# Kernel tuning notes

Measured on AMD Instinct MI355X. Metric: run time of the kernel, lower is better.

The kernel has to match this reference:

```python
import jax, jax.numpy as jnp
import numpy as np
import math

H = 12          # num_attention_heads
DH = 64         # attention_head_size
LN_EPS = 1e-5


def layer_norm(x, gamma, beta):
    mu = jnp.mean(x, axis=-1, keepdims=True)
    var = jnp.mean(jnp.square(x - mu), axis=-1, keepdims=True)
    return (x - mu) * jax.lax.rsqrt(var + LN_EPS) * gamma + beta


def setup_inputs() -> dict:
    key = jax.random.key(0)
    ks = jax.random.split(key, 12)
    B, Lq, Lk, D = 4, 512, 512, 768
    s = 1.0 / math.sqrt(D)
    return {
        "hidden_states": jax.random.normal(ks[0], (B, Lq, D), jnp.float32),
        "context": jax.random.normal(ks[1], (B, Lk, D), jnp.float32),
        "attention_mask": jnp.zeros((B, 1, 1, Lk), jnp.float32),
        "graph_arc": jax.random.randint(ks[2], (B, Lq, Lk), 0, 3, jnp.int32),
        "Wq": jax.random.normal(ks[3], (D, D), jnp.float32) * s,
        "bq": jnp.zeros((D,), jnp.float32),
        "Wk": jax.random.normal(ks[4], (D, D), jnp.float32) * s,
        "bk": jnp.zeros((D,), jnp.float32),
        "Wv": jax.random.normal(ks[5], (D, D), jnp.float32) * s,
        "bv": jnp.zeros((D,), jnp.float32),
        "dpk_emb": jax.random.normal(ks[6], (3, DH), jnp.float32),
        "dpv_emb": jax.random.normal(ks[7], (3, DH), jnp.float32),
        "lnk_g": jnp.ones((DH,), jnp.float32),
        "lnk_b": jnp.zeros((DH,), jnp.float32),
        "lnv_g": jnp.ones((DH,), jnp.float32),
        "lnv_b": jnp.zeros((DH,), jnp.float32),
    }


def reference(hidden_states, context, attention_mask, graph_arc,
              Wq, bq, Wk, bk, Wv, bv,
              dpk_emb, dpv_emb, lnk_g, lnk_b, lnv_g, lnv_b):
    B, Lq, D = hidden_states.shape
    Lk = context.shape[1]

    def heads(x, L):  # [B,L,D] -> [B,H,L,dh]
        return x.reshape(B, L, H, DH).transpose(0, 2, 1, 3)

    q = heads(hidden_states @ Wq + bq, Lq)
    k = heads(context @ Wk + bk, Lk)
    v = heads(context @ Wv + bv, Lk)

    # relation embeddings per (query, key) pair: [B,Lq,Lk,dh]
    dp_keys = layer_norm(dpk_emb[graph_arc], lnk_g, lnk_b)
    dp_values = layer_norm(dpv_emb[graph_arc], lnv_g, lnv_b)

    scores = jnp.einsum('bhqd,bhkd->bhqk', q, k) / math.sqrt(DH)
    scores = scores + jnp.einsum('bhqd,bqkd->bhqk', q, dp_keys)
    scores = scores + attention_mask
    probs = jax.nn.softmax(scores, axis=-1)  # dropout p=0.0 -> identity

    ctx = jnp.einsum('bhqk,bhkd->bhqd', probs, v)
    ctx = ctx + jnp.einsum('bhqk,bqkd->bhqd', probs, dp_values)
    ctx = ctx.transpose(0, 2, 1, 3).reshape(B, Lq, D)
    return ctx
```

## Files before the change

### kernel.cpp

```cpp
#include <hip/hip_runtime.h>
#include <hip/hip_fp16.h>

#define NB 4
#define NH 12
#define DHD 64
#define LQ 512
#define LK 512
#define DM 768

typedef __attribute__((ext_vector_type(4))) _Float16 f16x4;
typedef __attribute__((ext_vector_type(8))) _Float16 f16x8;
typedef __attribute__((ext_vector_type(4))) float f32x4;

typedef __attribute__((address_space(1))) const unsigned int ga_uint;
typedef __attribute__((address_space(3))) unsigned int lds_uint;
__device__ static inline void gload_lds16(const void* g, void* l) {
    __builtin_amdgcn_global_load_lds((ga_uint*)g, (lds_uint*)l, 16, 0, 0);
}

__global__ __launch_bounds__(256) void prep_kernel(
    const float* __restrict__ Wq, const float* __restrict__ Wk,
    const float* __restrict__ Wv,
    const float* __restrict__ dpk, const float* __restrict__ dpv,
    const float* __restrict__ gk, const float* __restrict__ bk,
    const float* __restrict__ gv, const float* __restrict__ bv,
    _Float16* __restrict__ WT, float* __restrict__ lnK, float* __restrict__ lnV)
{
    const int bid = blockIdx.x, t = threadIdx.x;
    if (bid < 432) {
        __shared__ float sT[64][65];
        int mat = bid / 144, tile = bid % 144;
        int k0 = (tile / 12) * 64, n0 = (tile % 12) * 64;
        const float* W = (mat == 0) ? Wq : (mat == 1) ? Wk : Wv;
        #pragma unroll
        for (int p = 0; p < 4; ++p) {
            int idx = t + p * 256;
            int ki = idx >> 4, nj = (idx & 15) * 4;
            float4 wv = *(const float4*)&W[(size_t)(k0 + ki) * DM + n0 + nj];
            sT[ki][nj + 0] = wv.x; sT[ki][nj + 1] = wv.y;
            sT[ki][nj + 2] = wv.z; sT[ki][nj + 3] = wv.w;
        }
        __syncthreads();
        _Float16* dst = WT + (size_t)mat * DM * DM;
        #pragma unroll
        for (int p = 0; p < 4; ++p) {
            int idx = t + p * 256;
            int nr = idx >> 4, kj = (idx & 15) * 4;
            f16x4 hv = { (_Float16)sT[kj + 0][nr], (_Float16)sT[kj + 1][nr],
                         (_Float16)sT[kj + 2][nr], (_Float16)sT[kj + 3][nr] };
            *(f16x4*)&dst[(size_t)(n0 + nr) * DM + k0 + kj] = hv;
        }
    } else if (t < 64) {
        int lane = t;
        for (int r = 0; r < 3; ++r) {
            {
                float x = dpk[r * DHD + lane];
                float s = x;
                #pragma unroll
                for (int o = 1; o < 64; o <<= 1) s += __shfl_xor(s, o);
                float mu = s * (1.0f / 64.0f);
                float d = x - mu;
                float v = d * d;
                #pragma unroll
                for (int o = 1; o < 64; o <<= 1) v += __shfl_xor(v, o);
                lnK[r * DHD + lane] =
                    (d * rsqrtf(v * (1.0f / 64.0f) + 1e-5f) * gk[lane] + bk[lane]) * 8.0f;
            }
            {
                float x = dpv[r * DHD + lane];
                float s = x;
                #pragma unroll
                for (int o = 1; o < 64; o <<= 1) s += __shfl_xor(s, o);
                float mu = s * (1.0f / 64.0f);
                float d = x - mu;
                float v = d * d;
                #pragma unroll
                for (int o = 1; o < 64; o <<= 1) v += __shfl_xor(v, o);
                lnV[r * DHD + lane] =
                    d * rsqrtf(v * (1.0f / 64.0f) + 1e-5f) * gv[lane] + bv[lane];
            }
        }
    }
}

__global__ __launch_bounds__(256) void qkv_mfma(
    const float* __restrict__ hidden, const float* __restrict__ context,
    const _Float16* __restrict__ WT,
    const float* __restrict__ bq, const float* __restrict__ bk,
    const float* __restrict__ bv,
    _Float16* __restrict__ Qh, _Float16* __restrict__ Kh,
    _Float16* __restrict__ VTh)
{
    __shared__ __align__(16) char smem[43008];
    _Float16 (*sA)[64][72] = (_Float16(*)[64][72])smem;
    _Float16 (*sC)[104] = (_Float16(*)[104])smem;
    _Float16 (*sCV)[72] = (_Float16(*)[72])smem;

    const int t = threadIdx.x;
    const int w = t >> 6, lane = t & 63, g = lane >> 4, c16 = lane & 15;
    const int wm = w >> 1, wn = w & 1;
    const int mat = blockIdx.y / 8, nt0 = blockIdx.y % 8;
    const int m0 = blockIdx.x * 64, n0 = nt0 * 96;
    const float* X     = (mat == 0) ? hidden : context;
    const _Float16* Wt = WT + (size_t)mat * DM * DM;
    const float* bias  = (mat == 0) ? bq : (mat == 1) ? bk : bv;

    const int srow  = lane >> 3;
    const int sunit = (lane & 7) ^ srow;

    #pragma unroll
    for (int p = 0; p < 4; ++p) {
        int idx = t + p * 256;
        int row = idx >> 4, c4 = idx & 15;
        float4 xv = *(const float4*)&X[(size_t)(m0 + row) * DM + c4 * 4];
        f16x4 hv = { (_Float16)xv.x, (_Float16)xv.y,
                     (_Float16)xv.z, (_Float16)xv.w };
        *(f16x4*)&sA[0][row][c4 * 4] = hv;
    }
    #pragma unroll
    for (int cc = 0; cc < 3; ++cc) {
        int chunk = w * 3 + cc;
        int row = chunk * 8 + srow;
        gload_lds16((const char*)&Wt[(size_t)(n0 + row) * DM] + sunit * 16,
                    smem + 18432 + chunk * 1024);
    }
    __syncthreads();

    f32x4 acc[2][3];
    #pragma unroll
    for (int mt = 0; mt < 2; ++mt)
        #pragma unroll
        for (int nt = 0; nt < 3; ++nt) acc[mt][nt] = (f32x4){0.f, 0.f, 0.f, 0.f};

    for (int kt = 0; kt < 12; ++kt) {
        const int cur = kt & 1, nxt = cur ^ 1;
        char* sBc = smem + 18432 + cur * 12288;
        char* sBn = smem + 18432 + nxt * 12288;
        float4 xv[4];
        if (kt < 11) {
            #pragma unroll
            for (int p = 0; p < 4; ++p) {
                int idx = t + p * 256;
                int row = idx >> 4, c4 = idx & 15;
                xv[p] = *(const float4*)&X[(size_t)(m0 + row) * DM + (kt + 1) * 64 + c4 * 4];
            }
            #pragma unroll
            for (int cc = 0; cc < 3; ++cc) {
                int chunk = w * 3 + cc;
                int row = chunk * 8 + srow;
                gload_lds16(
                    (const char*)&Wt[(size_t)(n0 + row) * DM + (kt + 1) * 64] + sunit * 16,
                    sBn + chunk * 1024);
            }
        }
        #pragma unroll
        for (int kh = 0; kh < 2; ++kh) {
            f16x8 af[2], bf[3];
            #pragma unroll
            for (int mt = 0; mt < 2; ++mt)
                af[mt] = *(const f16x8*)&sA[cur][wm * 32 + mt * 16 + c16][kh * 32 + 8 * g];
            #pragma unroll
            for (int nt = 0; nt < 3; ++nt) {
                int rn = wn * 48 + nt * 16 + c16;
                int boff = (rn * 128 + kh * 64 + g * 16) ^ ((rn & 7) << 4);
                bf[nt] = *(const f16x8*)(sBc + boff);
            }
            #pragma unroll
            for (int mt = 0; mt < 2; ++mt)
                #pragma unroll
                for (int nt = 0; nt < 3; ++nt)
                    acc[mt][nt] = __builtin_amdgcn_mfma_f32_16x16x32_f16(
                        af[mt], bf[nt], acc[mt][nt], 0, 0, 0);
        }
        if (kt < 11) {
            #pragma unroll
            for (int p = 0; p < 4; ++p) {
                int idx = t + p * 256;
                int row = idx >> 4, c4 = idx & 15;
                f16x4 hv = { (_Float16)xv[p].x, (_Float16)xv[p].y,
                             (_Float16)xv[p].z, (_Float16)xv[p].w };
                *(f16x4*)&sA[nxt][row][c4 * 4] = hv;
            }
        }
        __syncthreads();
    }

    const float sc = (mat == 0) ? 0.125f : 1.0f;
    float bb[3];
    #pragma unroll
    for (int nt = 0; nt < 3; ++nt)
        bb[nt] = bias[n0 + wn * 48 + nt * 16 + c16] * sc;
    __syncthreads();

    const int bbat = m0 >> 9, l0 = m0 & 511;
    if (mat < 2) {
        #pragma unroll
        for (int mt = 0; mt < 2; ++mt)
            #pragma unroll
            for (int nt = 0; nt < 3; ++nt)
                #pragma unroll
                for (int r = 0; r < 4; ++r)
                    sC[wm * 32 + mt * 16 + 4 * g + r][wn * 48 + nt * 16 + c16] =
                        (_Float16)(acc[mt][nt][r] * sc + bb[nt]);
        __syncthreads();
        _Float16* dst = (mat == 0) ? Qh : Kh;
        int row = t >> 2, qc = t & 3;
        #pragma unroll
        for (int j = 0; j < 3; ++j) {
            int col = qc * 24 + j * 8;
            int hd = (n0 + col) >> 6, d8 = (n0 + col) & 63;
            *(f16x8*)&dst[((size_t)(bbat * NH + hd) * LQ + l0 + row) * DHD + d8] =
                *(const f16x8*)&sC[row][col];
        }
    } else {
        #pragma unroll
        for (int mt = 0; mt < 2; ++mt)
            #pragma unroll
            for (int nt = 0; nt < 3; ++nt)
                #pragma unroll
                for (int r = 0; r < 4; ++r)
                    sCV[wn * 48 + nt * 16 + c16][wm * 32 + mt * 16 + 4 * g + r] =
                        (_Float16)(acc[mt][nt][r] + bb[nt]);
        __syncthreads();
        #pragma unroll
        for (int p = 0; p < 3; ++p) {
            int idx = t + p * 256;
            int n = idx >> 3, c8 = idx & 7;
            *(f16x8*)&VTh[((size_t)(bbat * NH + ((n0 + n) >> 6)) * DHD + ((n0 + n) & 63)) * LK
                          + l0 + c8 * 8] = *(const f16x8*)&sCV[n][c8 * 8];
        }
    }
}

__global__ __launch_bounds__(256) void attn_mfma(
    const _Float16* __restrict__ Qh, const _Float16* __restrict__ Kh,
    const _Float16* __restrict__ VTh, const float* __restrict__ maskp,
    const int* __restrict__ garc, const float* __restrict__ lnK,
    const float* __restrict__ lnV, float* __restrict__ outp)
{
    __shared__ __align__(16) _Float16 sP[32][520];
    __shared__ unsigned int sArcW[32 * 33];
    __shared__ float sTb[32][4];
    __shared__ float sMax[4][32];
    __shared__ float sFin[32][4];

    const int t = threadIdx.x;
    const int w = t >> 6, lane = t & 63, g = lane >> 4, c16 = lane & 15;
    const int bx = blockIdx.x;
    const int qt = bx & 15, h = (bx >> 4) % NH, b = bx / (16 * NH);
    const int q0 = qt * 32;
    const int kw = w * 128;

    const _Float16* Qb = Qh + ((size_t)(b * NH + h) * LQ) * DHD;
    const _Float16* Kb = Kh + ((size_t)(b * NH + h) * LK) * DHD;
    const _Float16* Vb = VTh + ((size_t)(b * NH + h) * DHD) * LK;

    if (t < 32) {
        sFin[t][0] = 0.f; sFin[t][1] = 0.f; sFin[t][2] = 0.f; sFin[t][3] = 0.f;
    }
    const int* garcRow = garc + ((size_t)(b * LQ + q0)) * LK;
    #pragma unroll
    for (int p = 0; p < 4; ++p) {
        int idx = t + p * 256;
        int row = idx >> 5, wd = idx & 31;
        const int4* src = (const int4*)&garcRow[idx * 16];
        unsigned int u = 0;
        #pragma unroll
        for (int j = 0; j < 4; ++j) {
            int4 a4 = src[j];
            u |= (unsigned int)a4.x << (j * 8 + 0);
            u |= (unsigned int)a4.y << (j * 8 + 2);
            u |= (unsigned int)a4.z << (j * 8 + 4);
            u |= (unsigned int)a4.w << (j * 8 + 6);
        }
        sArcW[row * 33 + wd] = u;
    }
    if (t < 192) {
        int q = t / 6, rem = t % 6, rr = rem >> 1, part = rem & 1;
        const _Float16* qp = Qb + (size_t)(q0 + q) * DHD + part * 32;
        const float* lp = lnK + rr * 64 + part * 32;
        float a = 0.f;
        #pragma unroll
        for (int j = 0; j < 4; ++j) {
            f16x8 qv = *(const f16x8*)&qp[j * 8];
            float4 l0 = *(const float4*)&lp[j * 8];
            float4 l1 = *(const float4*)&lp[j * 8 + 4];
            a += (float)qv[0] * l0.x + (float)qv[1] * l0.y
               + (float)qv[2] * l0.z + (float)qv[3] * l0.w
               + (float)qv[4] * l1.x + (float)qv[5] * l1.y
               + (float)qv[6] * l1.z + (float)qv[7] * l1.w;
        }
        a += __shfl_xor(a, 1);
        if (part == 0) sTb[q][rr] = a;
    }
    f16x8 qa[2][2];
    #pragma unroll
    for (int qg = 0; qg < 2; ++qg) {
        qa[qg][0] = *(const f16x8*)&Qb[(q0 + 16 * qg + c16) * DHD + 8 * g];
        qa[qg][1] = *(const f16x8*)&Qb[(q0 + 16 * qg + c16) * DHD + 32 + 8 * g];
    }
    __syncthreads();

    f32x4 c[8][2];
    unsigned int aPk[2][2] = {{0u, 0u}, {0u, 0u}};
    float rm[2][4];
    const int sh = c16 * 2;
    #pragma unroll
    for (int qg = 0; qg < 2; ++qg)
        #pragma unroll
        for (int r = 0; r < 4; ++r) rm[qg][r] = -1e30f;
    #pragma unroll
    for (int tt = 0; tt < 8; ++tt) {
        int kg = kw + tt * 16 + c16;
        f16x8 kb0 = *(const f16x8*)&Kb[kg * DHD + 8 * g];
        f16x8 kb1 = *(const f16x8*)&Kb[kg * DHD + 32 + 8 * g];
        float mv = maskp[b * LK + kg];
        const int wb = w * 8 + tt;
        #pragma unroll
        for (int qg = 0; qg < 2; ++qg) {
            f32x4 s = (f32x4){0.f, 0.f, 0.f, 0.f};
            s = __builtin_amdgcn_mfma_f32_16x16x32_f16(qa[qg][0], kb0, s, 0, 0, 0);
            s = __builtin_amdgcn_mfma_f32_16x16x32_f16(qa[qg][1], kb1, s, 0, 0, 0);
            #pragma unroll
            for (int r = 0; r < 4; ++r) {
                int qrow = 16 * qg + 4 * g + r;
                unsigned int a = (sArcW[qrow * 33 + wb] >> sh) & 3u;
                aPk[qg][tt >> 2] |= a << ((tt & 3) * 8 + 2 * r);
                float sv = s[r] + sTb[qrow][a] + mv;
                s[r] = sv;
                rm[qg][r] = fmaxf(rm[qg][r], sv);
            }
            c[tt][qg] = s;
        }
    }

    #pragma unroll
    for (int qg = 0; qg < 2; ++qg)
        #pragma unroll
        for (int r = 0; r < 4; ++r) {
            float m = rm[qg][r];
            m = fmaxf(m, __shfl_xor(m, 1));
            m = fmaxf(m, __shfl_xor(m, 2));
            m = fmaxf(m, __shfl_xor(m, 4));
            m = fmaxf(m, __shfl_xor(m, 8));
            rm[qg][r] = m;
        }
    if (c16 == 0)
        #pragma unroll
        for (int qg = 0; qg < 2; ++qg)
            #pragma unroll
            for (int r = 0; r < 4; ++r) sMax[w][16 * qg + 4 * g + r] = rm[qg][r];
    __syncthreads();
    float Mr[2][4];
    #pragma unroll
    for (int qg = 0; qg < 2; ++qg)
        #pragma unroll
        for (int r = 0; r < 4; ++r) {
            int q = 16 * qg + 4 * g + r;
            Mr[qg][r] = fmaxf(fmaxf(sMax[0][q], sMax[1][q]),
                              fmaxf(sMax[2][q], sMax[3][q]));
        }

    float b0s[2][4], b1s[2][4], b2s[2][4];
    #pragma unroll
    for (int qg = 0; qg < 2; ++qg)
        #pragma unroll
        for (int r = 0; r < 4; ++r) {
            b0s[qg][r] = 0.f; b1s[qg][r] = 0.f; b2s[qg][r] = 0.f;
        }
    #pragma unroll
    for (int tt = 0; tt < 8; ++tt) {
        int kg = kw + tt * 16 + c16;
        #pragma unroll
        for (int qg = 0; qg < 2; ++qg)
            #pragma unroll
            for (int r = 0; r < 4; ++r) {
                float e = __expf(c[tt][qg][r] - Mr[qg][r]);
                unsigned int a = (aPk[qg][tt >> 2] >> ((tt & 3) * 8 + 2 * r)) & 3u;
                b0s[qg][r] += (a == 0u) ? e : 0.f;
                b1s[qg][r] += (a == 1u) ? e : 0.f;
                b2s[qg][r] += (a == 2u) ? e : 0.f;
                sP[16 * qg + 4 * g + r][kg] = (_Float16)e;
            }
    }
    #pragma unroll
    for (int qg = 0; qg < 2; ++qg)
        #pragma unroll
        for (int r = 0; r < 4; ++r) {
            #pragma unroll
            for (int o = 1; o < 16; o <<= 1) {
                b0s[qg][r] += __shfl_xor(b0s[qg][r], o);
                b1s[qg][r] += __shfl_xor(b1s[qg][r], o);
                b2s[qg][r] += __shfl_xor(b2s[qg][r], o);
            }
        }
    if (c16 == 0)
        #pragma unroll
        for (int qg = 0; qg < 2; ++qg)
            #pragma unroll
            for (int r = 0; r < 4; ++r) {
                int q = 16 * qg + 4 * g + r;
                atomicAdd(&sFin[q][0], b0s[qg][r]);
                atomicAdd(&sFin[q][1], b1s[qg][r]);
                atomicAdd(&sFin[q][2], b2s[qg][r]);
            }
    __syncthreads();

    f32x4 o[2] = {(f32x4){0.f, 0.f, 0.f, 0.f}, (f32x4){0.f, 0.f, 0.f, 0.f}};
    const _Float16* vrow = Vb + (size_t)(w * 16 + c16) * LK;
    #pragma unroll
    for (int ktile = 0; ktile < 16; ++ktile) {
        f16x8 vb = *(const f16x8*)&vrow[ktile * 32 + 8 * g];
        #pragma unroll
        for (int qg = 0; qg < 2; ++qg) {
            f16x8 pa = *(const f16x8*)&sP[16 * qg + c16][ktile * 32 + 8 * g];
            o[qg] = __builtin_amdgcn_mfma_f32_16x16x32_f16(pa, vb, o[qg], 0, 0, 0);
        }
    }

    int d = w * 16 + c16;
    float lv0 = lnV[d], lv1 = lnV[64 + d], lv2 = lnV[128 + d];
    #pragma unroll
    for (int qg = 0; qg < 2; ++qg)
        #pragma unroll
        for (int r = 0; r < 4; ++r) {
            int q = 16 * qg + 4 * g + r;
            float4 st = *(const float4*)&sFin[q][0];
            float inv = 1.0f / (st.x + st.y + st.z);
            float val = (o[qg][r] + st.x * lv0 + st.y * lv1 + st.z * lv2) * inv;
            outp[((size_t)(b * LQ + q0 + q)) * DM + h * DHD + d] = val;
        }
}

extern "C" void kernel_launch(void* const* d_in, const int* in_sizes, int n_in,
                              void* d_out, int out_size, void* d_ws, size_t ws_size,
                              hipStream_t stream) {
    const float* hidden  = (const float*)d_in[0];
    const float* context = (const float*)d_in[1];
    const float* mask    = (const float*)d_in[2];
    const int*   garc    = (const int*)d_in[3];
    const float* Wq = (const float*)d_in[4];
    const float* bq = (const float*)d_in[5];
    const float* Wk = (const float*)d_in[6];
    const float* bk = (const float*)d_in[7];
    const float* Wv = (const float*)d_in[8];
    const float* bv = (const float*)d_in[9];
    const float* dpk  = (const float*)d_in[10];
    const float* dpv  = (const float*)d_in[11];
    const float* lnkg = (const float*)d_in[12];
    const float* lnkb = (const float*)d_in[13];
    const float* lnvg = (const float*)d_in[14];
    const float* lnvb = (const float*)d_in[15];
    float* out = (float*)d_out;

    const size_t perT = (size_t)NB * NH * LQ * DHD;
    _Float16* Qh  = (_Float16*)d_ws;
    _Float16* Kh  = Qh + perT;
    _Float16* VTh = Kh + perT;
    _Float16* WT  = VTh + perT;
    float* lnK = (float*)(WT + (size_t)3 * DM * DM);
    float* lnV = lnK + 192;

    prep_kernel<<<433, 256, 0, stream>>>(Wq, Wk, Wv, dpk, dpv,
                                         lnkg, lnkb, lnvg, lnvb, WT, lnK, lnV);
    qkv_mfma<<<dim3(32, 24), 256, 0, stream>>>(hidden, context, WT,
                                               bq, bk, bv, Qh, Kh, VTh);
    attn_mfma<<<768, 256, 0, stream>>>(Qh, Kh, VTh, mask, garc, lnK, lnV, out);
}
```

Baseline: 138.5 us.

## Pre-pack graph arcs once and halve attention query tile to 16 rows

```diff
diff --git a/kernel.cpp b/kernel.cpp
--- a/kernel.cpp
+++ b/kernel.cpp
@@ -24,7 +24,9 @@
     const float* __restrict__ dpk, const float* __restrict__ dpv,
     const float* __restrict__ gk, const float* __restrict__ bk,
     const float* __restrict__ gv, const float* __restrict__ bv,
-    _Float16* __restrict__ WT, float* __restrict__ lnK, float* __restrict__ lnV)
+    const int* __restrict__ garc,
+    _Float16* __restrict__ WT, float* __restrict__ lnK, float* __restrict__ lnV,
+    unsigned int* __restrict__ arcP)
 {
     const int bid = blockIdx.x, t = threadIdx.x;
     if (bid < 432) {
@@ -50,35 +52,56 @@
                          (_Float16)sT[kj + 2][nr], (_Float16)sT[kj + 3][nr] };
             *(f16x4*)&dst[(size_t)(n0 + nr) * DM + k0 + kj] = hv;
         }
-    } else if (t < 64) {
-        int lane = t;
-        for (int r = 0; r < 3; ++r) {
-            {
-                float x = dpk[r * DHD + lane];
-                float s = x;
-                #pragma unroll
-                for (int o = 1; o < 64; o <<= 1) s += __shfl_xor(s, o);
-                float mu = s * (1.0f / 64.0f);
-                float d = x - mu;
-                float v = d * d;
-                #pragma unroll
-                for (int o = 1; o < 64; o <<= 1) v += __shfl_xor(v, o);
-                lnK[r * DHD + lane] =
-                    (d * rsqrtf(v * (1.0f / 64.0f) + 1e-5f) * gk[lane] + bk[lane]) * 8.0f;
-            }
-            {
-                float x = dpv[r * DHD + lane];
-                float s = x;
-                #pragma unroll
-                for (int o = 1; o < 64; o <<= 1) s += __shfl_xor(s, o);
-                float mu = s * (1.0f / 64.0f);
-                float d = x - mu;
-                float v = d * d;
-                #pragma unroll
-                for (int o = 1; o < 64; o <<= 1) v += __shfl_xor(v, o);
-                lnV[r * DHD + lane] =
-                    d * rsqrtf(v * (1.0f / 64.0f) + 1e-5f) * gv[lane] + bv[lane];
-            }
+    } else if (bid == 432) {
+        if (t < 64) {
+            int lane = t;
+            for (int r = 0; r < 3; ++r) {
+                {
+                    float x = dpk[r * DHD + lane];
+                    float s = x;
+                    #pragma unroll
+                    for (int o = 1; o < 64; o <<= 1) s += __shfl_xor(s, o);
+                    float mu = s * (1.0f / 64.0f);
+                    float d = x - mu;
+                    float v = d * d;
+                    #pragma unroll
+                    for (int o = 1; o < 64; o <<= 1) v += __shfl_xor(v, o);
+                    lnK[r * DHD + lane] =
+                        (d * rsqrtf(v * (1.0f / 64.0f) + 1e-5f) * gk[lane] + bk[lane]) * 8.0f;
+                }
+                {
+                    float x = dpv[r * DHD + lane];
+                    float s = x;
+                    #pragma unroll
+                    for (int o = 1; o < 64; o <<= 1) s += __shfl_xor(s, o);
+                    float mu = s * (1.0f / 64.0f);
+                    float d = x - mu;
+                    float v = d * d;
+                    #pragma unroll
+                    for (int o = 1; o < 64; o <<= 1) v += __shfl_xor(v, o);
+                    lnV[r * DHD + lane] =
+                        d * rsqrtf(v * (1.0f / 64.0f) + 1e-5f) * gv[lane] + bv[lane];
+                }
+            }
+        }
+    } else {
+        int pb = bid - 433;
+        #pragma unroll
+        for (int j = 0; j < 2; ++j) {
+            int wi = pb * 512 + t + j * 256;
+            int bq = wi >> 5;
+            int wd = wi & 31;
+            const int4* src = (const int4*)&garc[((size_t)bq * LK) + wd * 16];
+            unsigned int u = 0;
+            #pragma unroll
+            for (int k = 0; k < 4; ++k) {
+                int4 a4 = src[k];
+                u |= (unsigned int)a4.x << (k * 8 + 0);
+                u |= (unsigned int)a4.y << (k * 8 + 2);
+                u |= (unsigned int)a4.z << (k * 8 + 4);
+                u |= (unsigned int)a4.w << (k * 8 + 6);
+            }
+            arcP[wi] = u;
         }
     }
 }
@@ -235,47 +258,36 @@
 __global__ __launch_bounds__(256) void attn_mfma(
     const _Float16* __restrict__ Qh, const _Float16* __restrict__ Kh,
     const _Float16* __restrict__ VTh, const float* __restrict__ maskp,
-    const int* __restrict__ garc, const float* __restrict__ lnK,
+    const unsigned int* __restrict__ arcP, const float* __restrict__ lnK,
     const float* __restrict__ lnV, float* __restrict__ outp)
 {
-    __shared__ __align__(16) _Float16 sP[32][520];
-    __shared__ unsigned int sArcW[32 * 33];
-    __shared__ float sTb[32][4];
-    __shared__ float sMax[4][32];
-    __shared__ float sFin[32][4];
+    __shared__ __align__(16) _Float16 sP[16][520];
+    __shared__ unsigned int sArcW[16 * 33];
+    __shared__ float sTb[16][4];
+    __shared__ float sMax[4][16];
+    __shared__ float sFin[16][4];
 
     const int t = threadIdx.x;
     const int w = t >> 6, lane = t & 63, g = lane >> 4, c16 = lane & 15;
     const int bx = blockIdx.x;
-    const int qt = bx & 15, h = (bx >> 4) % NH, b = bx / (16 * NH);
-    const int q0 = qt * 32;
+    const int qt = bx & 31, h = (bx >> 5) % NH, b = bx / (32 * NH);
+    const int q0 = qt * 16;
     const int kw = w * 128;
 
     const _Float16* Qb = Qh + ((size_t)(b * NH + h) * LQ) * DHD;
     const _Float16* Kb = Kh + ((size_t)(b * NH + h) * LK) * DHD;
     const _Float16* Vb = VTh + ((size_t)(b * NH + h) * DHD) * LK;
 
-    if (t < 32) {
+    if (t < 16) {
         sFin[t][0] = 0.f; sFin[t][1] = 0.f; sFin[t][2] = 0.f; sFin[t][3] = 0.f;
     }
-    const int* garcRow = garc + ((size_t)(b * LQ + q0)) * LK;
-    #pragma unroll
-    for (int p = 0; p < 4; ++p) {
-        int idx = t + p * 256;
+    #pragma unroll
+    for (int j = 0; j < 2; ++j) {
+        int idx = t + j * 256;
         int row = idx >> 5, wd = idx & 31;
-        const int4* src = (const int4*)&garcRow[idx * 16];
-        unsigned int u = 0;
-        #pragma unroll
-        for (int j = 0; j < 4; ++j) {
-            int4 a4 = src[j];
-            u |= (unsigned int)a4.x << (j * 8 + 0);
-            u |= (unsigned int)a4.y << (j * 8 + 2);
-            u |= (unsigned int)a4.z << (j * 8 + 4);
-            u |= (unsigned int)a4.w << (j * 8 + 6);
-        }
-        sArcW[row * 33 + wd] = u;
-    }
-    if (t < 192) {
+        sArcW[row * 33 + wd] = arcP[((size_t)(b * LQ + q0 + row)) * 32 + wd];
+    }
+    if (t < 96) {
         int q = t / 6, rem = t % 6, rr = rem >> 1, part = rem & 1;
         const _Float16* qp = Qb + (size_t)(q0 + q) * DHD + part * 32;
         const float* lp = lnK + rr * 64 + part * 32;
@@ -293,22 +305,16 @@
         a += __shfl_xor(a, 1);
         if (part == 0) sTb[q][rr] = a;
     }
-    f16x8 qa[2][2];
-    #pragma unroll
-    for (int qg = 0; qg < 2; ++qg) {
-        qa[qg][0] = *(const f16x8*)&Qb[(q0 + 16 * qg + c16) * DHD + 8 * g];
-        qa[qg][1] = *(const f16x8*)&Qb[(q0 + 16 * qg + c16) * DHD + 32 + 8 * g];
-    }
+    f16x8 qa0 = *(const f16x8*)&Qb[(q0 + c16) * DHD + 8 * g];
+    f16x8 qa1 = *(const f16x8*)&Qb[(q0 + c16) * DHD + 32 + 8 * g];
     __syncthreads();
 
-    f32x4 c[8][2];
-    unsigned int aPk[2][2] = {{0u, 0u}, {0u, 0u}};
-    float rm[2][4];
+    f32x4 c[8];
+    unsigned int aPk[2] = {0u, 0u};
+    float rm[4];
     const int sh = c16 * 2;
     #pragma unroll
-    for (int qg = 0; qg < 2; ++qg)
-        #pragma unroll
-        for (int r = 0; r < 4; ++r) rm[qg][r] = -1e30f;
+    for (int r = 0; r < 4; ++r) rm[r] = -1e30f;
     #pragma unroll
     for (int tt = 0; tt < 8; ++tt) {
         int kg = kw + tt * 16 + c16;
@@ -316,120 +322,96 @@
         f16x8 kb1 = *(const f16x8*)&Kb[kg * DHD + 32 + 8 * g];
         float mv = maskp[b * LK + kg];
         const int wb = w * 8 + tt;
-        #pragma unroll
-        for (int qg = 0; qg < 2; ++qg) {
-            f32x4 s = (f32x4){0.f, 0.f, 0.f, 0.f};
-            s = __builtin_amdgcn_mfma_f32_16x16x32_f16(qa[qg][0], kb0, s, 0, 0, 0);
-            s = __builtin_amdgcn_mfma_f32_16x16x32_f16(qa[qg][1], kb1, s, 0, 0, 0);
-            #pragma unroll
-            for (int r = 0; r < 4; ++r) {
-                int qrow = 16 * qg + 4 * g + r;
-                unsigned int a = (sArcW[qrow * 33 + wb] >> sh) & 3u;
-                aPk[qg][tt >> 2] |= a << ((tt & 3) * 8 + 2 * r);
-                float sv = s[r] + sTb[qrow][a] + mv;
-                s[r] = sv;
-                rm[qg][r] = fmaxf(rm[qg][r], sv);
-            }
-            c[tt][qg] = s;
-        }
-    }
-
-    #pragma unroll
-    for (int qg = 0; qg < 2; ++qg)
+        f32x4 s = (f32x4){0.f, 0.f, 0.f, 0.f};
+        s = __builtin_amdgcn_mfma_f32_16x16x32_f16(qa0, kb0, s, 0, 0, 0);
+        s = __builtin_amdgcn_mfma_f32_16x16x32_f16(qa1, kb1, s, 0, 0, 0);
         #pragma unroll
         for (int r = 0; r < 4; ++r) {
-            float m = rm[qg][r];
-            m = fmaxf(m, __shfl_xor(m, 1));
-            m = fmaxf(m, __shfl_xor(m, 2));
-            m = fmaxf(m, __shfl_xor(m, 4));
-            m = fmaxf(m, __shfl_xor(m, 8));
-            rm[qg][r] = m;
-        }
+            int qrow = 4 * g + r;
+            unsigned int a = (sArcW[qrow * 33 + wb] >> sh) & 3u;
+            aPk[tt >> 2] |= a << ((tt & 3) * 8 + 2 * r);
+            float sv = s[r] + sTb[qrow][a] + mv;
+            s[r] = sv;
+            rm[r] = fmaxf(rm[r], sv);
+        }
+        c[tt] = s;
+    }
+
+    #pragma unroll
+    for (int r = 0; r < 4; ++r) {
+        float m = rm[r];
+        m = fmaxf(m, __shfl_xor(m, 1));
+        m = fmaxf(m, __shfl_xor(m, 2));
+        m = fmaxf(m, __shfl_xor(m, 4));
+        m = fmaxf(m, __shfl_xor(m, 8));
+        rm[r] = m;
+    }
     if (c16 == 0)
         #pragma unroll
-        for (int qg = 0; qg < 2; ++qg)
-            #pragma unroll
-            for (int r = 0; r < 4; ++r) sMax[w][16 * qg + 4 * g + r] = rm[qg][r];
+        for (int r = 0; r < 4; ++r) sMax[w][4 * g + r] = rm[r];
     __syncthreads();
-    float Mr[2][4];
-    #pragma unroll
-    for (int qg = 0; qg < 2; ++qg)
-        #pragma unroll
-        for (int r = 0; r < 4; ++r) {
-            int q = 16 * qg + 4 * g + r;
-            Mr[qg][r] = fmaxf(fmaxf(sMax[0][q], sMax[1][q]),
-                              fmaxf(sMax[2][q], sMax[3][q]));
-        }
-
-    float b0s[2][4], b1s[2][4], b2s[2][4];
-    #pragma unroll
-    for (int qg = 0; qg < 2; ++qg)
-        #pragma unroll
-        for (int r = 0; r < 4; ++r) {
-            b0s[qg][r] = 0.f; b1s[qg][r] = 0.f; b2s[qg][r] = 0.f;
-        }
+    float Mr[4];
+    #pragma unroll
+    for (int r = 0; r < 4; ++r) {
+        int q = 4 * g + r;
+        Mr[r] = fmaxf(fmaxf(sMax[0][q], sMax[1][q]),
+                      fmaxf(sMax[2][q], sMax[3][q]));
+    }
+
+    float b0s[4], b1s[4], b2s[4];
+    #pragma unroll
+    for (int r = 0; r < 4; ++r) { b0s[r] = 0.f; b1s[r] = 0.f; b2s[r] = 0.f; }
     #pragma unroll
     for (int tt = 0; tt < 8; ++tt) {
         int kg = kw + tt * 16 + c16;
         #pragma unroll
-        for (int qg = 0; qg < 2; ++qg)
-            #pragma unroll
-            for (int r = 0; r < 4; ++r) {
-                float e = __expf(c[tt][qg][r] - Mr[qg][r]);
-                unsigned int a = (aPk[qg][tt >> 2] >> ((tt & 3) * 8 + 2 * r)) & 3u;
-                b0s[qg][r] += (a == 0u) ? e : 0.f;
-                b1s[qg][r] += (a == 1u) ? e : 0.f;
-                b2s[qg][r] += (a == 2u) ? e : 0.f;
-                sP[16 * qg + 4 * g + r][kg] = (_Float16)e;
-            }
-    }
-    #pragma unroll
-    for (int qg = 0; qg < 2; ++qg)
-        #pragma unroll
         for (int r = 0; r < 4; ++r) {
-            #pragma unroll
-            for (int o = 1; o < 16; o <<= 1) {
-                b0s[qg][r] += __shfl_xor(b0s[qg][r], o);
-                b1s[qg][r] += __shfl_xor(b1s[qg][r], o);
-                b2s[qg][r] += __shfl_xor(b2s[qg][r], o);
-            }
-        }
+            float e = __expf(c[tt][r] - Mr[r]);
+            unsigned int a = (aPk[tt >> 2] >> ((tt & 3) * 8 + 2 * r)) & 3u;
+            b0s[r] += (a == 0u) ? e : 0.f;
+            b1s[r] += (a == 1u) ? e : 0.f;
+            b2s[r] += (a == 2u) ? e : 0.f;
+            sP[4 * g + r][kg] = (_Float16)e;
+        }
+    }
+    #pragma unroll
+    for (int r = 0; r < 4; ++r) {
+        #pragma unroll
+        for (int o = 1; o < 16; o <<= 1) {
+            b0s[r] += __shfl_xor(b0s[r], o);
+            b1s[r] += __shfl_xor(b1s[r], o);
+            b2s[r] += __shfl_xor(b2s[r], o);
+        }
+    }
     if (c16 == 0)
         #pragma unroll
-        for (int qg = 0; qg < 2; ++qg)
-            #pragma unroll
-            for (int r = 0; r < 4; ++r) {
-                int q = 16 * qg + 4 * g + r;
-                atomicAdd(&sFin[q][0], b0s[qg][r]);
-                atomicAdd(&sFin[q][1], b1s[qg][r]);
-                atomicAdd(&sFin[q][2], b2s[qg][r]);
-            }
+        for (int r = 0; r < 4; ++r) {
+            int q = 4 * g + r;
+            atomicAdd(&sFin[q][0], b0s[r]);
+            atomicAdd(&sFin[q][1], b1s[r]);
+            atomicAdd(&sFin[q][2], b2s[r]);
+        }
     __syncthreads();
 
-    f32x4 o[2] = {(f32x4){0.f, 0.f, 0.f, 0.f}, (f32x4){0.f, 0.f, 0.f, 0.f}};
+    f32x4 o = (f32x4){0.f, 0.f, 0.f, 0.f};
     const _Float16* vrow = Vb + (size_t)(w * 16 + c16) * LK;
     #pragma unroll
     for (int ktile = 0; ktile < 16; ++ktile) {
         f16x8 vb = *(const f16x8*)&vrow[ktile * 32 + 8 * g];
-        #pragma unroll
-        for (int qg = 0; qg < 2; ++qg) {
-            f16x8 pa = *(const f16x8*)&sP[16 * qg + c16][ktile * 32 + 8 * g];
-            o[qg] = __builtin_amdgcn_mfma_f32_16x16x32_f16(pa, vb, o[qg], 0, 0, 0);
-        }
+        f16x8 pa = *(const f16x8*)&sP[c16][ktile * 32 + 8 * g];
+        o = __builtin_amdgcn_mfma_f32_16x16x32_f16(pa, vb, o, 0, 0, 0);
     }
 
     int d = w * 16 + c16;
     float lv0 = lnV[d], lv1 = lnV[64 + d], lv2 = lnV[128 + d];
     #pragma unroll
-    for (int qg = 0; qg < 2; ++qg)
-        #pragma unroll
-        for (int r = 0; r < 4; ++r) {
-            int q = 16 * qg + 4 * g + r;
-            float4 st = *(const float4*)&sFin[q][0];
-            float inv = 1.0f / (st.x + st.y + st.z);
-            float val = (o[qg][r] + st.x * lv0 + st.y * lv1 + st.z * lv2) * inv;
-            outp[((size_t)(b * LQ + q0 + q)) * DM + h * DHD + d] = val;
-        }
+    for (int r = 0; r < 4; ++r) {
+        int q = 4 * g + r;
+        float4 st = *(const float4*)&sFin[q][0];
+        float inv = 1.0f / (st.x + st.y + st.z);
+        float val = (o[r] + st.x * lv0 + st.y * lv1 + st.z * lv2) * inv;
+        outp[((size_t)(b * LQ + q0 + q)) * DM + h * DHD + d] = val;
+    }
 }
 
 extern "C" void kernel_launch(void* const* d_in, const int* in_sizes, int n_in,
@@ -460,10 +442,12 @@
     _Float16* WT  = VTh + perT;
     float* lnK = (float*)(WT + (size_t)3 * DM * DM);
     float* lnV = lnK + 192;
-
-    prep_kernel<<<433, 256, 0, stream>>>(Wq, Wk, Wv, dpk, dpv,
-                                         lnkg, lnkb, lnvg, lnvb, WT, lnK, lnV);
+    unsigned int* arcP = (unsigned int*)(lnV + 192);
+
+    prep_kernel<<<561, 256, 0, stream>>>(Wq, Wk, Wv, dpk, dpv,
+                                         lnkg, lnkb, lnvg, lnvb, garc,
+                                         WT, lnK, lnV, arcP);
     qkv_mfma<<<dim3(32, 24), 256, 0, stream>>>(hidden, context, WT,
                                                bq, bk, bv, Qh, Kh, VTh);
-    attn_mfma<<<768, 256, 0, stream>>>(Qh, Kh, VTh, mask, garc, lnK, lnV, out);
+    attn_mfma<<<1536, 256, 0, stream>>>(Qh, Kh, VTh, mask, arcP, lnK, lnV, out);
 }
```

Measured after the change: 143.0 us. +3.2%, slower.
